# Performance work log

Measured on AMD Instinct MI355X. Metric: run time of the kernel, lower is better.

## Reference

```python
import jax, jax.numpy as jnp
import numpy as np

V, D, L, H, HD, FF, E, K, B, S = 32000, 768, 4, 12, 64, 2048, 8, 2, 2, 512
EPS = 1e-6
SCALE = HD ** -0.5


def rmsnorm(x, w):
    return w * x * jax.lax.rsqrt(jnp.mean(x * x, axis=-1, keepdims=True) + EPS)


def attention(x, wq, wk, wv, wo):
    # x: [B,S,D]
    q = jnp.einsum('bsd,de->bse', x, wq).reshape(B, S, H, HD)
    k = jnp.einsum('bsd,de->bse', x, wk).reshape(B, S, H, HD)
    v = jnp.einsum('bsd,de->bse', x, wv).reshape(B, S, H, HD)
    scores = jnp.einsum('bqhd,bkhd->bhqk', q, k) * SCALE
    a = jax.nn.softmax(scores, axis=-1)
    out = jnp.einsum('bhqk,bkhd->bqhd', a, v).reshape(B, S, D)
    return out @ wo


def moe(x, rw, gw, uw, dw):
    # x: [T,D]; rw: [D,E]; gw/uw: [E,D,FF]; dw: [E,FF,D]
    probs = jax.nn.softmax(x @ rw, axis=-1)            # [T,E]
    topv, topi = jax.lax.top_k(probs, K)               # [T,K]
    topv = topv / jnp.sum(topv, axis=-1, keepdims=True)
    combine = jnp.einsum('tke,tk->te', jax.nn.one_hot(topi, E, dtype=x.dtype), topv)  # [T,E]
    g = jnp.einsum('td,edf->etf', x, gw)               # [E,T,FF]
    u = jnp.einsum('td,edf->etf', x, uw)
    eo = jnp.einsum('etf,efd->etd', jax.nn.silu(g) * u, dw)  # [E,T,D]
    return jnp.einsum('etd,te->td', eo, combine)


def setup_inputs() -> dict:
    key = jax.random.key(0)
    ks = jax.random.split(key, 12)
    p = lambda k, shape: 0.02 * jax.random.normal(k, shape, jnp.float32)
    return {
        'input_ids': jax.random.randint(ks[0], (B, S), 0, V),
        'embed_tokens': p(ks[1], (V, D)),
        'embed_pos': p(ks[2], (S, D)),
        'wq': p(ks[3], (L, D, D)),
        'wk': p(ks[4], (L, D, D)),
        'wv': p(ks[5], (L, D, D)),
        'wo': p(ks[6], (L, D, D)),
        'norm1_w': jnp.ones((L, D), jnp.float32),
        'norm2_w': jnp.ones((L, D), jnp.float32),
        'router_w': p(ks[7], (L, D, E)),
        'gate_w': p(ks[8], (L, E, D, FF)),
        'up_w': p(ks[9], (L, E, D, FF)),
        'down_w': p(ks[10], (L, E, FF, D)),
        'final_norm_w': jnp.ones((D,), jnp.float32),
        'lm_head_w': p(ks[11], (D, V)),
    }


def reference(input_ids, embed_tokens, embed_pos, wq, wk, wv, wo, norm1_w, norm2_w,
              router_w, gate_w, up_w, down_w, final_norm_w, lm_head_w):
    x = embed_tokens[input_ids] + embed_pos[None, :, :]   # [B,S,D]
    for l in range(L):
        x = x + attention(rmsnorm(x, norm1_w[l]), wq[l], wk[l], wv[l], wo[l])
        t = rmsnorm(x, norm2_w[l]).reshape(-1, D)
        x = x + moe(t, router_w[l], gate_w[l], up_w[l], down_w[l]).reshape(B, S, D)
    logits = rmsnorm(x, final_norm_w) @ lm_head_w        # [B,S,V]
    return logits
```

## Files before the change

kernel.cpp:

```cpp
#include <hip/hip_runtime.h>
#include <math.h>

#define TT   1024
#define DM   768
#define NH   12
#define HD   64
#define FFD  2048
#define NE   8
#define SQ   512
#define NB   2
#define NL   4
#define NV   32000
#define REPS 1e-6f
#define QB   16
#define LMC  3200

typedef float f32x4 __attribute__((ext_vector_type(4)));
typedef short s16x8 __attribute__((ext_vector_type(8)));

__device__ __forceinline__ float b2f(ushort u) {
  return __uint_as_float(((unsigned)u) << 16);
}
__device__ __forceinline__ ushort f2b(float f) {
  unsigned i = __float_as_uint(f);
  return (ushort)((i + 0x7FFFu + ((i >> 16) & 1u)) >> 16);
}

__global__ __launch_bounds__(256) void k_embed(const int* __restrict__ ids,
    const float* __restrict__ tok, const float* __restrict__ pos, float* __restrict__ x) {
  int t = blockIdx.x; int s = t % SQ; int id = ids[t];
  for (int d = threadIdx.x; d < DM; d += 256)
    x[t * DM + d] = tok[(size_t)id * DM + d] + pos[s * DM + d];
}

__global__ __launch_bounds__(64) void k_router(const float* __restrict__ xn,
    const float* __restrict__ rw, int* __restrict__ topi, float* __restrict__ topw,
    int* __restrict__ posb, int* __restrict__ slot, int* __restrict__ counts) {
  int t = blockIdx.x, l = threadIdx.x;
  float acc[NE] = {};
  for (int d = l; d < DM; d += 64) {
    float xv = xn[t * DM + d];
    const float* r = &rw[d * NE];
#pragma unroll
    for (int e = 0; e < NE; ++e) acc[e] += xv * r[e];
  }
#pragma unroll
  for (int off = 32; off > 0; off >>= 1)
#pragma unroll
    for (int e = 0; e < NE; ++e) acc[e] += __shfl_down(acc[e], off, 64);
  if (l == 0) {
    float mx = acc[0];
#pragma unroll
    for (int e = 1; e < NE; ++e) mx = fmaxf(mx, acc[e]);
    float p[NE], sum = 0.f;
#pragma unroll
    for (int e = 0; e < NE; ++e) { p[e] = expf(acc[e] - mx); sum += p[e]; }
#pragma unroll
    for (int e = 0; e < NE; ++e) p[e] /= sum;
    int i0 = 0;
    for (int e = 1; e < NE; ++e) if (p[e] > p[i0]) i0 = e;
    int i1 = (i0 == 0) ? 1 : 0;
    for (int e = 0; e < NE; ++e) if (e != i0 && p[e] > p[i1]) i1 = e;
    float w0 = p[i0], w1 = p[i1], inv = 1.f / (w0 + w1);
    w0 *= inv; w1 *= inv;
    int p0 = atomicAdd(&counts[i0], 1);
    int p1 = atomicAdd(&counts[i1], 1);
    topi[2 * t] = i0; topi[2 * t + 1] = i1;
    topw[2 * t] = w0; topw[2 * t + 1] = w1;
    posb[2 * t] = p0; posb[2 * t + 1] = p1;
    slot[i0 * TT + p0] = t; slot[i1 * TT + p1] = t;
  }
}

__global__ void k_zero8(int* c) { if (threadIdx.x < NE) c[threadIdx.x] = 0; }

__global__ void k_offsets(const int* __restrict__ counts, int* __restrict__ off) {
  int a = 0;
  for (int e = 0; e < NE; ++e) { off[e] = a; a += counts[e]; }
  off[NE] = a;
}

__global__ __launch_bounds__(256) void k_combine(const float* __restrict__ eo,
    const int* __restrict__ topi, const float* __restrict__ topw,
    const int* __restrict__ posb, const int* __restrict__ offs, float* __restrict__ x) {
  int t = blockIdx.x;
  int r0 = offs[topi[2 * t]] + posb[2 * t];
  int r1 = offs[topi[2 * t + 1]] + posb[2 * t + 1];
  float w0 = topw[2 * t], w1 = topw[2 * t + 1];
  for (int d = threadIdx.x; d < DM; d += 256)
    x[t * DM + d] += w0 * eo[(size_t)r0 * DM + d] + w1 * eo[(size_t)r1 * DM + d];
}

__global__ __launch_bounds__(256) void k_attn2(const float* __restrict__ qkv,
    float* __restrict__ O) {
  __shared__ float Qs[QB][64];
  __shared__ float KVs[128][68];
  __shared__ float sc[QB][516];
  __shared__ float red[256];
  __shared__ float mrow[QB], invr[QB];
  int qt = blockIdx.x, h = blockIdx.y, b = blockIdx.z;
  int tid = threadIdx.x;
  int q0 = qt * QB;
  const float* base = qkv + (size_t)(b * SQ) * (3 * DM);
  {
    int qi = tid >> 4, d4 = (tid & 15) * 4;
    *(float4*)&Qs[qi][d4] = *(const float4*)&base[(size_t)(q0 + qi) * (3 * DM) + h * HD + d4];
  }
  for (int kt = 0; kt < 4; ++kt) {
    __syncthreads();
    {
      int kk = tid >> 4, d4 = (tid & 15) * 4;
#pragma unroll
      for (int i = 0; i < 8; ++i)
        *(float4*)&KVs[kk + 16 * i][d4] =
            *(const float4*)&base[(size_t)(kt * 128 + kk + 16 * i) * (3 * DM) + DM + h * HD + d4];
    }
    __syncthreads();
    int q2 = tid >> 5, k4 = tid & 31;
    float a0[4] = {}, a1[4] = {};
#pragma unroll
    for (int i = 0; i < 16; ++i) {
      float4 qa = *(float4*)&Qs[2 * q2][4 * i];
      float4 qb = *(float4*)&Qs[2 * q2 + 1][4 * i];
#pragma unroll
      for (int j = 0; j < 4; ++j) {
        float4 kv = *(float4*)&KVs[k4 + 32 * j][4 * i];
        a0[j] += qa.x * kv.x + qa.y * kv.y + qa.z * kv.z + qa.w * kv.w;
        a1[j] += qb.x * kv.x + qb.y * kv.y + qb.z * kv.z + qb.w * kv.w;
      }
    }
#pragma unroll
    for (int j = 0; j < 4; ++j) {
      sc[2 * q2][kt * 128 + 32 * j + k4] = a0[j] * 0.125f;
      sc[2 * q2 + 1][kt * 128 + 32 * j + k4] = a1[j] * 0.125f;
    }
  }
  __syncthreads();
  int row = tid & 15, seg = tid >> 4;
  float m = -1e30f;
  for (int i = 0; i < 32; ++i) m = fmaxf(m, sc[row][seg + 16 * i]);
  red[tid] = m; __syncthreads();
  if (tid < QB) {
    float mm = red[tid];
#pragma unroll
    for (int j = 1; j < 16; ++j) mm = fmaxf(mm, red[tid + 16 * j]);
    mrow[tid] = mm;
  }
  __syncthreads();
  m = mrow[row];
  float s = 0.f;
  for (int i = 0; i < 32; ++i) {
    int c = seg + 16 * i;
    float e = expf(sc[row][c] - m);
    sc[row][c] = e; s += e;
  }
  red[tid] = s; __syncthreads();
  if (tid < QB) {
    float ss = red[tid];
#pragma unroll
    for (int j = 1; j < 16; ++j) ss += red[tid + 16 * j];
    invr[tid] = 1.0f / ss;
  }
  float4 o = {0.f, 0.f, 0.f, 0.f};
  int q = tid >> 4, d4 = (tid & 15) * 4;
  for (int vt = 0; vt < 4; ++vt) {
    __syncthreads();
    {
      int kk = tid >> 4, dd = (tid & 15) * 4;
#pragma unroll
      for (int i = 0; i < 8; ++i)
        *(float4*)&KVs[kk + 16 * i][dd] =
            *(const float4*)&base[(size_t)(vt * 128 + kk + 16 * i) * (3 * DM) + 2 * DM + h * HD + dd];
    }
    __syncthreads();
    for (int kk = 0; kk < 128; ++kk) {
      float w = sc[q][vt * 128 + kk];
      float4 v = *(float4*)&KVs[kk][d4];
      o.x += w * v.x; o.y += w * v.y; o.z += w * v.z; o.w += w * v.w;
    }
  }
  float iv = invr[q];
  o.x *= iv; o.y *= iv; o.z *= iv; o.w *= iv;
  *(float4*)&O[(size_t)(b * SQ + q0 + q) * DM + h * HD + d4] = o;
}

__global__ __launch_bounds__(256) void k_rmsnorm_sb(const float* __restrict__ x,
    const float* __restrict__ w, float* __restrict__ y,
    ushort* __restrict__ yh, ushort* __restrict__ yl) {
  __shared__ float red[256];
  int t = blockIdx.x, tid = threadIdx.x;
  float ss = 0.f;
  for (int d = tid; d < DM; d += 256) { float v = x[t * DM + d]; ss += v * v; }
  red[tid] = ss; __syncthreads();
  for (int s = 128; s > 0; s >>= 1) { if (tid < s) red[tid] += red[tid + s]; __syncthreads(); }
  float inv = 1.0f / sqrtf(red[0] / (float)DM + REPS);
  for (int d = tid; d < DM; d += 256) {
    float v = w[d] * x[t * DM + d] * inv;
    ushort h = f2b(v);
    y[t * DM + d] = v;
    yh[t * DM + d] = h;
    yl[t * DM + d] = f2b(v - b2f(h));
  }
}

__global__ __launch_bounds__(256) void k_split(const float* __restrict__ in,
    ushort* __restrict__ oh, ushort* __restrict__ ol) {
  int t = blockIdx.x;
  for (int d = threadIdx.x; d < DM; d += 256) {
    float v = in[(size_t)t * DM + d];
    ushort h = f2b(v);
    oh[(size_t)t * DM + d] = h;
    ol[(size_t)t * DM + d] = f2b(v - b2f(h));
  }
}

__global__ __launch_bounds__(256) void k_rmsnorm_b(const float* __restrict__ x,
    const float* __restrict__ w, ushort* __restrict__ y) {
  __shared__ float red[256];
  int t = blockIdx.x, tid = threadIdx.x;
  float ss = 0.f;
  for (int d = tid; d < DM; d += 256) { float v = x[t * DM + d]; ss += v * v; }
  red[tid] = ss; __syncthreads();
  for (int s = 128; s > 0; s >>= 1) { if (tid < s) red[tid] += red[tid + s]; __syncthreads(); }
  float inv = 1.0f / sqrtf(red[0] / (float)DM + REPS);
  for (int d = tid; d < DM; d += 256)
    y[t * DM + d] = f2b(w[d] * x[t * DM + d] * inv);
}

__global__ __launch_bounds__(256) void k_tconv(const float* __restrict__ in,
    ushort* __restrict__ out, int K, int ns, int mode) {
  __shared__ float tile[32][33];
  int n0 = blockIdx.x * 32, k0 = blockIdx.y * 32;
  int c = threadIdx.x & 31, rq = threadIdx.x >> 5;
#pragma unroll
  for (int rr = rq; rr < 32; rr += 8)
    tile[rr][c] = in[(size_t)(k0 + rr) * ns + n0 + c];
  __syncthreads();
#pragma unroll
  for (int rr = rq; rr < 32; rr += 8) {
    int n = n0 + rr;
    int orow = (mode == 0) ? n : (((n >> 4) << 5) + ((mode == 1) ? 0 : 16) + (n & 15));
    out[(size_t)orow * K + k0 + c] = f2b(tile[c][rr]);
  }
}

#define EPI_RES  1
#define EPI_F32  2
#define EPI_GU   3
#define EPI_DOWN 4
#define MODE_B   0
#define MODE_QKV 1
#define MODE_GU  2

template<int EPI, int RM>
__global__ __launch_bounds__(256) void k_gmm(
    const ushort* __restrict__ A, const ushort* __restrict__ Bt,
    ushort* __restrict__ Cb, float* __restrict__ Cf,
    int M, int K, int ldc, int e_arg,
    const int* __restrict__ slot, const int* __restrict__ counts,
    const int* __restrict__ offs) {
  (void)e_arg; (void)slot; (void)counts; (void)offs; (void)Cb;
  int cnt = M;
  int m0 = blockIdx.y * 128;
  if (m0 >= cnt) return;
  int n0 = blockIdx.x * 128;
  __shared__ __align__(16) ushort As[128 * 40];
  __shared__ __align__(16) ushort Bs[128 * 40];
  int tid = threadIdx.x;
  int lane = tid & 63;
  int wave = tid >> 6;
  int wr = wave >> 1, wc = wave & 1;
  int ar1 = tid >> 2, ar2 = ar1 + 64, kc = tid & 3;
  const ushort* Arow1 = A + (size_t)(m0 + ar1) * K;
  const ushort* Arow2 = A + (size_t)(m0 + ar2) * K;
  const ushort* Brow1 = Bt + (size_t)(n0 + ar1) * K;
  const ushort* Brow2 = Bt + (size_t)(n0 + ar2) * K;
  f32x4 zr = {0.f, 0.f, 0.f, 0.f};
  f32x4 acc[4][4];
#pragma unroll
  for (int i = 0; i < 4; ++i)
#pragma unroll
    for (int j = 0; j < 4; ++j) acc[i][j] = zr;
  int rl = lane & 15, g = lane >> 4;
  for (int k0 = 0; k0 < K; k0 += 32) {
    s16x8 va1 = *(const s16x8*)(Arow1 + k0 + kc * 8);
    s16x8 va2 = *(const s16x8*)(Arow2 + k0 + kc * 8);
    s16x8 vb1 = *(const s16x8*)(Brow1 + k0 + kc * 8);
    s16x8 vb2 = *(const s16x8*)(Brow2 + k0 + kc * 8);
    __syncthreads();
    *(s16x8*)&As[ar1 * 40 + kc * 8] = va1;
    *(s16x8*)&As[ar2 * 40 + kc * 8] = va2;
    *(s16x8*)&Bs[ar1 * 40 + kc * 8] = vb1;
    *(s16x8*)&Bs[ar2 * 40 + kc * 8] = vb2;
    __syncthreads();
    s16x8 av[4], bv[4];
#pragma unroll
    for (int mi = 0; mi < 4; ++mi)
      av[mi] = *(const s16x8*)&As[(wr * 64 + mi * 16 + rl) * 40 + g * 8];
#pragma unroll
    for (int ni = 0; ni < 4; ++ni)
      bv[ni] = *(const s16x8*)&Bs[(wc * 64 + ni * 16 + rl) * 40 + g * 8];
#pragma unroll
    for (int mi = 0; mi < 4; ++mi)
#pragma unroll
      for (int ni = 0; ni < 4; ++ni)
        acc[mi][ni] = __builtin_amdgcn_mfma_f32_16x16x32_bf16(av[mi], bv[ni], acc[mi][ni], 0, 0, 0);
  }
  int rg4 = (lane >> 4) * 4;
#pragma unroll
  for (int mi = 0; mi < 4; ++mi)
#pragma unroll
    for (int rg = 0; rg < 4; ++rg) {
      int rloc = m0 + wr * 64 + mi * 16 + rg4 + rg;
#pragma unroll
      for (int ni = 0; ni < 4; ++ni)
        Cf[(size_t)rloc * ldc + n0 + wc * 64 + ni * 16 + rl] = acc[mi][ni][rg];
    }
}

template<int BM, int BN, int MODE, int EPI, int RM, int SK, int NBX, int PREC>
__global__ __launch_bounds__(256) void k_gmm2(
    const ushort* __restrict__ Ah, const ushort* __restrict__ Al,
    const float* __restrict__ B0, const float* __restrict__ B1, const float* __restrict__ B2,
    long long bstride, ushort* __restrict__ Ch, ushort* __restrict__ Cl,
    float* __restrict__ Cf, float* __restrict__ Cf2,
    int M, int K, int ldb, int ldc,
    const int* __restrict__ slot, const int* __restrict__ counts,
    const int* __restrict__ offs) {
  constexpr int NEg  = (RM == 0) ? 1 : NE;
  constexpr int P    = NBX * NEg * SK;
  constexpr int Ppad = ((P + 7) / 8) * 8;
  int id = blockIdx.x;
  int m = id / Ppad, pp = id % Ppad;
  if (pp >= P) return;
  int e = pp / (NBX * SK);
  int rr = pp % (NBX * SK);
  int x = rr / SK, sk = rr % SK;

  int cnt = (RM == 0) ? M : counts[e];
  int m0 = m * BM;
  if (m0 >= cnt) return;
  int n0 = x * BN;
  int off = (RM == 0) ? 0 : offs[e];
  int KK = K / SK, kbeg = sk * KK;

  constexpr int WM = (BM == 128) ? 64 : ((BN == 128) ? 64 : 32);
  constexpr int WN = (BM == 128) ? 64 : 32;
  constexpr int MI = WM / 16, NI = WN / 16;

  __shared__ __align__(16) ushort Ahs[BM * 40];
  __shared__ __align__(16) ushort Als[(PREC == 2) ? BM * 40 : 16];
  __shared__ __align__(16) ushort Bhs[BN * 40];
  __shared__ __align__(16) ushort Bls[(PREC == 2) ? BN * 40 : 16];

  int tid = threadIdx.x;
  int wave = tid >> 6, lane = tid & 63;
  int wr, wc;
  if (BM == 128)      { wr = wave >> 1; wc = wave & 1; }
  else if (BN == 128) { wr = 0;         wc = wave;     }
  else                { wr = wave >> 1; wc = wave & 1; }
  int moff;
  if (BM == 64 && BN == 128) moff = 0; else moff = wr * ((BM == 128) ? 64 : 32);
  int noff = wc * WN;

  int arA = tid >> 2, kcA = tid & 3;
  int ar1 = tid >> 2, ar2 = ar1 + 64;
  size_t aoff1 = 0, aoff2 = 0;
  if (BM == 64) {
    int rowi;
    if (RM == 0)      rowi = m0 + arA;
    else if (RM == 1) rowi = slot[e * TT + min(m0 + arA, cnt - 1)];
    else              rowi = off + min(m0 + arA, cnt - 1);
    aoff1 = (size_t)rowi * K;
  } else {
    if (RM == 0) {
      aoff1 = (size_t)(m0 + ar1) * K;
      aoff2 = (size_t)(m0 + ar2) * K;
    } else if (RM == 1) {
      aoff1 = (size_t)slot[e * TT + min(m0 + ar1, cnt - 1)] * K;
      aoff2 = (size_t)slot[e * TT + min(m0 + ar2, cnt - 1)] * K;
    } else {
      aoff1 = (size_t)(off + min(m0 + ar1, cnt - 1)) * K;
      aoff2 = (size_t)(off + min(m0 + ar2, cnt - 1)) * K;
    }
  }

  int rB = tid & 63, ko = tid >> 6;
  auto bcol = [&](int r) -> const float* {
    if (MODE == MODE_QKV) {
      int mat = x / (NBX / 3);
      const float* Bm = (mat == 0) ? B0 : ((mat == 1) ? B1 : B2);
      return Bm + (x % (NBX / 3)) * BN + r;
    } else if (MODE == MODE_GU) {
      const float* Bg = B0 + (size_t)e * bstride;
      const float* Bu = B1 + (size_t)e * bstride;
      return ((((r) >> 4) & 1) ? Bu : Bg) + x * (BN / 2) + ((((r) >> 5) << 4) | ((r) & 15));
    }
    return B0 + (size_t)e * bstride + n0 + r;
  };
  const float* bs0 = bcol(rB);
  const float* bs1 = (BN == 128) ? bcol(rB + 64) : nullptr;

  s16x8 rah1, rah2, ral1, ral2;
  float vb0[8], vb1[8];

  auto loadA = [&](int kk) {
    if (BM == 64) {
      rah1 = *(const s16x8*)(Ah + aoff1 + kbeg + kk + kcA * 8);
      if (PREC == 2) ral1 = *(const s16x8*)(Al + aoff1 + kbeg + kk + kcA * 8);
    } else {
      rah1 = *(const s16x8*)(Ah + aoff1 + kbeg + kk + kcA * 8);
      rah2 = *(const s16x8*)(Ah + aoff2 + kbeg + kk + kcA * 8);
      if (PREC == 2) {
        ral1 = *(const s16x8*)(Al + aoff1 + kbeg + kk + kcA * 8);
        ral2 = *(const s16x8*)(Al + aoff2 + kbeg + kk + kcA * 8);
      }
    }
  };
  auto loadB = [&](int kk) {
#pragma unroll
    for (int i = 0; i < 8; ++i)
      vb0[i] = bs0[(size_t)(kbeg + kk + ko * 8 + i) * ldb];
    if (BN == 128) {
#pragma unroll
      for (int i = 0; i < 8; ++i)
        vb1[i] = bs1[(size_t)(kbeg + kk + ko * 8 + i) * ldb];
    }
  };
  auto storeLDS = [&]() {
    if (BM == 64) {
      *(s16x8*)&Ahs[arA * 40 + kcA * 8] = rah1;
      if (PREC == 2) *(s16x8*)&Als[arA * 40 + kcA * 8] = ral1;
    } else {
      *(s16x8*)&Ahs[ar1 * 40 + kcA * 8] = rah1;
      *(s16x8*)&Ahs[ar2 * 40 + kcA * 8] = rah2;
      if (PREC == 2) {
        *(s16x8*)&Als[ar1 * 40 + kcA * 8] = ral1;
        *(s16x8*)&Als[ar2 * 40 + kcA * 8] = ral2;
      }
    }
    s16x8 h0, l0;
#pragma unroll
    for (int i = 0; i < 8; ++i) {
      ushort h = f2b(vb0[i]);
      h0[i] = (short)h;
      if (PREC == 2) l0[i] = (short)f2b(vb0[i] - b2f(h));
    }
    *(s16x8*)&Bhs[rB * 40 + ko * 8] = h0;
    if (PREC == 2) *(s16x8*)&Bls[rB * 40 + ko * 8] = l0;
    if (BN == 128) {
      s16x8 h1, l1;
#pragma unroll
      for (int i = 0; i < 8; ++i) {
        ushort h = f2b(vb1[i]);
        h1[i] = (short)h;
        if (PREC == 2) l1[i] = (short)f2b(vb1[i] - b2f(h));
      }
      *(s16x8*)&Bhs[(rB + 64) * 40 + ko * 8] = h1;
      if (PREC == 2) *(s16x8*)&Bls[(rB + 64) * 40 + ko * 8] = l1;
    }
  };

  f32x4 zr = {0.f, 0.f, 0.f, 0.f};
  f32x4 acc[MI][NI];
#pragma unroll
  for (int i = 0; i < MI; ++i)
#pragma unroll
    for (int j = 0; j < NI; ++j) acc[i][j] = zr;

  int rl = lane & 15, g = lane >> 4;
  loadA(0); loadB(0);
  for (int k0 = 0; k0 < KK; k0 += 32) {
    __syncthreads();
    storeLDS();
    __syncthreads();
    if (k0 + 32 < KK) { loadA(k0 + 32); loadB(k0 + 32); }
#pragma unroll
    for (int mi = 0; mi < MI; ++mi) {
      int ra = (moff + mi * 16 + rl) * 40 + g * 8;
      s16x8 avh = *(const s16x8*)&Ahs[ra];
      s16x8 avl;
      if (PREC == 2) avl = *(const s16x8*)&Als[ra];
#pragma unroll
      for (int ni = 0; ni < NI; ++ni) {
        int rb = (noff + ni * 16 + rl) * 40 + g * 8;
        s16x8 bvh = *(const s16x8*)&Bhs[rb];
        f32x4 a = acc[mi][ni];
        if (PREC == 2) {
          s16x8 bvl = *(const s16x8*)&Bls[rb];
          a = __builtin_amdgcn_mfma_f32_16x16x32_bf16(avl, bvh, a, 0, 0, 0);
          a = __builtin_amdgcn_mfma_f32_16x16x32_bf16(avh, bvl, a, 0, 0, 0);
        }
        a = __builtin_amdgcn_mfma_f32_16x16x32_bf16(avh, bvh, a, 0, 0, 0);
        acc[mi][ni] = a;
      }
    }
  }

  float* Cfx = (SK == 2 && sk == 1) ? Cf2 : Cf;
  int rg4 = (lane >> 4) * 4;
#pragma unroll
  for (int mi = 0; mi < MI; ++mi) {
#pragma unroll
    for (int rg = 0; rg < 4; ++rg) {
      int rloc = m0 + moff + mi * 16 + rg4 + rg;
      if ((EPI == EPI_GU || EPI == EPI_DOWN) && rloc >= cnt) continue;
      if (EPI == EPI_GU) {
        float gv = acc[mi][0][rg], uv = acc[mi][1][rg];
        float hv = gv / (1.f + __expf(-gv)) * uv;
        int fq = (n0 + noff) >> 5;
        size_t ix = (size_t)(off + rloc) * ldc + fq * 16 + rl;
        ushort h = f2b(hv);
        Ch[ix] = h;
        Cl[ix] = f2b(hv - b2f(h));
      } else if (EPI == EPI_RES) {
#pragma unroll
        for (int ni = 0; ni < NI; ++ni) {
          size_t ix = (size_t)rloc * ldc + n0 + noff + ni * 16 + rl;
          Cf[ix] += acc[mi][ni][rg];
        }
      } else if (EPI == EPI_F32) {
#pragma unroll
        for (int ni = 0; ni < NI; ++ni)
          Cfx[(size_t)rloc * ldc + n0 + noff + ni * 16 + rl] = acc[mi][ni][rg];
      } else {
#pragma unroll
        for (int ni = 0; ni < NI; ++ni)
          Cfx[(size_t)(off + rloc) * ldc + n0 + noff + ni * 16 + rl] = acc[mi][ni][rg];
      }
    }
  }
}

extern "C" void kernel_launch(void* const* d_in, const int* in_sizes, int n_in,
                              void* d_out, int out_size, void* d_ws, size_t ws_size,
                              hipStream_t stream) {
  (void)in_sizes; (void)n_in; (void)out_size; (void)ws_size;
  const int*   ids = (const int*)d_in[0];
  const float* tok = (const float*)d_in[1];
  const float* pos = (const float*)d_in[2];
  const float* wq  = (const float*)d_in[3];
  const float* wk  = (const float*)d_in[4];
  const float* wv  = (const float*)d_in[5];
  const float* wo  = (const float*)d_in[6];
  const float* n1w = (const float*)d_in[7];
  const float* n2w = (const float*)d_in[8];
  const float* rw  = (const float*)d_in[9];
  const float* gw  = (const float*)d_in[10];
  const float* uw  = (const float*)d_in[11];
  const float* dw  = (const float*)d_in[12];
  const float* fnw = (const float*)d_in[13];
  const float* lmw = (const float*)d_in[14];
  float* out = (float*)d_out;

  char* p = (char*)d_ws;
  auto alloc = [&](size_t bytes) { char* r = p; p += (bytes + 255) & ~(size_t)255; return r; };
  float*  x    = (float*)alloc((size_t)TT * DM * 4);
  float*  xn   = (float*)alloc((size_t)TT * DM * 4);
  ushort* xh   = (ushort*)alloc((size_t)TT * DM * 2);
  ushort* xl   = (ushort*)alloc((size_t)TT * DM * 2);
  float*  qkv  = (float*)alloc((size_t)TT * 3 * DM * 4);
  float*  ao   = (float*)alloc((size_t)TT * DM * 4);
  ushort* aoh  = (ushort*)alloc((size_t)TT * DM * 2);
  ushort* aol  = (ushort*)alloc((size_t)TT * DM * 2);
  ushort* Hh   = (ushort*)alloc((size_t)2 * TT * FFD * 2);
  ushort* Hl   = (ushort*)alloc((size_t)2 * TT * FFD * 2);
  float*  eo   = (float*)alloc((size_t)2 * TT * DM * 4);
  float*  topw = (float*)alloc((size_t)2 * TT * 4);
  int* topi    = (int*)alloc((size_t)2 * TT * 4);
  int* posb    = (int*)alloc((size_t)2 * TT * 4);
  int* slot    = (int*)alloc((size_t)NE * TT * 4);
  int* counts  = (int*)alloc(256);
  int* offs    = (int*)alloc(256);
  ushort* wlm  = (ushort*)alloc((size_t)LMC * DM * 2);
  ushort* xnb  = (ushort*)alloc((size_t)TT * DM * 2);

  k_embed<<<TT, 256, 0, stream>>>(ids, tok, pos, x);
  for (int l = 0; l < NL; ++l) {
    k_rmsnorm_sb<<<TT, 256, 0, stream>>>(x, n1w + l * DM, xn, xh, xl);
    k_gmm2<64, 64, MODE_QKV, EPI_F32, 0, 1, 36, 2><<<16 * 40, 256, 0, stream>>>(
        xh, xl, wq + (size_t)l * DM * DM, wk + (size_t)l * DM * DM, wv + (size_t)l * DM * DM,
        0, nullptr, nullptr, qkv, nullptr, TT, DM, DM, 3 * DM, nullptr, nullptr, nullptr);
    k_attn2<<<dim3(SQ / QB, NH, NB), 256, 0, stream>>>(qkv, ao);
    k_split<<<TT, 256, 0, stream>>>(ao, aoh, aol);
    k_gmm2<64, 64, MODE_B, EPI_RES, 0, 1, 12, 2><<<16 * 16, 256, 0, stream>>>(
        aoh, aol, wo + (size_t)l * DM * DM, nullptr, nullptr,
        0, nullptr, nullptr, x, nullptr, TT, DM, DM, DM, nullptr, nullptr, nullptr);

    k_rmsnorm_sb<<<TT, 256, 0, stream>>>(x, n2w + l * DM, xn, xh, xl);
    k_zero8<<<1, 64, 0, stream>>>(counts);
    k_router<<<TT, 64, 0, stream>>>(xn, rw + (size_t)l * DM * NE, topi, topw, posb, slot, counts);
    k_offsets<<<1, 1, 0, stream>>>(counts, offs);
    k_gmm2<64, 128, MODE_GU, EPI_GU, 1, 1, 32, 2><<<16 * 256, 256, 0, stream>>>(
        xh, xl, gw + (size_t)l * NE * DM * FFD, uw + (size_t)l * NE * DM * FFD, nullptr,
        (long long)DM * FFD, Hh, Hl, nullptr, nullptr, TT, DM, FFD, FFD, slot, counts, offs);
    k_gmm2<64, 64, MODE_B, EPI_DOWN, 2, 1, 12, 2><<<16 * 96, 256, 0, stream>>>(
        Hh, Hl, dw + (size_t)l * NE * FFD * DM, nullptr, nullptr,
        (long long)FFD * DM, nullptr, nullptr, eo, nullptr, TT, FFD, DM, DM, slot, counts, offs);
    k_combine<<<TT, 256, 0, stream>>>(eo, topi, topw, posb, offs, x);
  }

  k_rmsnorm_b<<<TT, 256, 0, stream>>>(x, fnw, xnb);
  for (int c = 0; c < NV / LMC; ++c) {
    k_tconv<<<dim3(LMC / 32, 24), 256, 0, stream>>>(lmw + c * LMC, wlm, DM, NV, 0);
    k_gmm<EPI_F32, 0><<<dim3(LMC / 128, 8), 256, 0, stream>>>(
        xnb, wlm, nullptr, out + c * LMC, TT, DM, NV, 0, nullptr, nullptr, nullptr);
  }
}
```

Baseline: 1.650 ms.

## Fuse split into attention, drop tiny kernels, single-pass LM head GEMM

The attention kernel now writes bf16 hi/lo outputs directly, so the separate split kernel and its fp32 round-trip go away. The counts zeroing moves into the rmsnorm kernel, and the expert offsets are computed inline from counts inside the GEMM and combine kernels, removing two single-block launches. The LM head drops the 10-chunk transpose-convert plus GEMM loop in favour of one k_gmm2 launch that reads the fp32 weights directly in single-bf16 precision, with a column-major block decode. Split-K support is removed from k_gmm2.

```diff
diff --git a/kernel.cpp b/kernel.cpp
--- a/kernel.cpp
+++ b/kernel.cpp
@@ -13,7 +13,6 @@
 #define NV   32000
 #define REPS 1e-6f
 #define QB   16
-#define LMC  3200
 
 typedef float f32x4 __attribute__((ext_vector_type(4)));
 typedef short s16x8 __attribute__((ext_vector_type(8)));
@@ -72,27 +71,22 @@
   }
 }
 
-__global__ void k_zero8(int* c) { if (threadIdx.x < NE) c[threadIdx.x] = 0; }
-
-__global__ void k_offsets(const int* __restrict__ counts, int* __restrict__ off) {
-  int a = 0;
-  for (int e = 0; e < NE; ++e) { off[e] = a; a += counts[e]; }
-  off[NE] = a;
-}
-
 __global__ __launch_bounds__(256) void k_combine(const float* __restrict__ eo,
     const int* __restrict__ topi, const float* __restrict__ topw,
-    const int* __restrict__ posb, const int* __restrict__ offs, float* __restrict__ x) {
+    const int* __restrict__ posb, const int* __restrict__ counts, float* __restrict__ x) {
   int t = blockIdx.x;
-  int r0 = offs[topi[2 * t]] + posb[2 * t];
-  int r1 = offs[topi[2 * t + 1]] + posb[2 * t + 1];
+  int pre[NE]; int a = 0;
+#pragma unroll
+  for (int e = 0; e < NE; ++e) { pre[e] = a; a += counts[e]; }
+  int r0 = pre[topi[2 * t]] + posb[2 * t];
+  int r1 = pre[topi[2 * t + 1]] + posb[2 * t + 1];
   float w0 = topw[2 * t], w1 = topw[2 * t + 1];
   for (int d = threadIdx.x; d < DM; d += 256)
     x[t * DM + d] += w0 * eo[(size_t)r0 * DM + d] + w1 * eo[(size_t)r1 * DM + d];
 }
 
 __global__ __launch_bounds__(256) void k_attn2(const float* __restrict__ qkv,
-    float* __restrict__ O) {
+    ushort* __restrict__ aoh, ushort* __restrict__ aol) {
   __shared__ float Qs[QB][64];
   __shared__ float KVs[128][68];
   __shared__ float sc[QB][516];
@@ -180,15 +174,22 @@
     }
   }
   float iv = invr[q];
-  o.x *= iv; o.y *= iv; o.z *= iv; o.w *= iv;
-  *(float4*)&O[(size_t)(b * SQ + q0 + q) * DM + h * HD + d4] = o;
+  size_t ob = (size_t)(b * SQ + q0 + q) * DM + h * HD + d4;
+  float ov[4] = {o.x * iv, o.y * iv, o.z * iv, o.w * iv};
+#pragma unroll
+  for (int j = 0; j < 4; ++j) {
+    ushort hh = f2b(ov[j]);
+    aoh[ob + j] = hh;
+    aol[ob + j] = f2b(ov[j] - b2f(hh));
+  }
 }
 
 __global__ __launch_bounds__(256) void k_rmsnorm_sb(const float* __restrict__ x,
     const float* __restrict__ w, float* __restrict__ y,
-    ushort* __restrict__ yh, ushort* __restrict__ yl) {
+    ushort* __restrict__ yh, ushort* __restrict__ yl, int* __restrict__ zc) {
   __shared__ float red[256];
   int t = blockIdx.x, tid = threadIdx.x;
+  if (zc && t == 0 && tid < NE) zc[tid] = 0;
   float ss = 0.f;
   for (int d = tid; d < DM; d += 256) { float v = x[t * DM + d]; ss += v * v; }
   red[tid] = ss; __syncthreads();
@@ -203,17 +204,6 @@
   }
 }
 
-__global__ __launch_bounds__(256) void k_split(const float* __restrict__ in,
-    ushort* __restrict__ oh, ushort* __restrict__ ol) {
-  int t = blockIdx.x;
-  for (int d = threadIdx.x; d < DM; d += 256) {
-    float v = in[(size_t)t * DM + d];
-    ushort h = f2b(v);
-    oh[(size_t)t * DM + d] = h;
-    ol[(size_t)t * DM + d] = f2b(v - b2f(h));
-  }
-}
-
 __global__ __launch_bounds__(256) void k_rmsnorm_b(const float* __restrict__ x,
     const float* __restrict__ w, ushort* __restrict__ y) {
   __shared__ float red[256];
@@ -227,23 +217,6 @@
     y[t * DM + d] = f2b(w[d] * x[t * DM + d] * inv);
 }
 
-__global__ __launch_bounds__(256) void k_tconv(const float* __restrict__ in,
-    ushort* __restrict__ out, int K, int ns, int mode) {
-  __shared__ float tile[32][33];
-  int n0 = blockIdx.x * 32, k0 = blockIdx.y * 32;
-  int c = threadIdx.x & 31, rq = threadIdx.x >> 5;
-#pragma unroll
-  for (int rr = rq; rr < 32; rr += 8)
-    tile[rr][c] = in[(size_t)(k0 + rr) * ns + n0 + c];
-  __syncthreads();
-#pragma unroll
-  for (int rr = rq; rr < 32; rr += 8) {
-    int n = n0 + rr;
-    int orow = (mode == 0) ? n : (((n >> 4) << 5) + ((mode == 1) ? 0 : 16) + (n & 15));
-    out[(size_t)orow * K + k0 + c] = f2b(tile[c][rr]);
-  }
-}
-
 #define EPI_RES  1
 #define EPI_F32  2
 #define EPI_GU   3
@@ -252,97 +225,35 @@
 #define MODE_QKV 1
 #define MODE_GU  2
 
-template<int EPI, int RM>
-__global__ __launch_bounds__(256) void k_gmm(
-    const ushort* __restrict__ A, const ushort* __restrict__ Bt,
-    ushort* __restrict__ Cb, float* __restrict__ Cf,
-    int M, int K, int ldc, int e_arg,
-    const int* __restrict__ slot, const int* __restrict__ counts,
-    const int* __restrict__ offs) {
-  (void)e_arg; (void)slot; (void)counts; (void)offs; (void)Cb;
-  int cnt = M;
-  int m0 = blockIdx.y * 128;
-  if (m0 >= cnt) return;
-  int n0 = blockIdx.x * 128;
-  __shared__ __align__(16) ushort As[128 * 40];
-  __shared__ __align__(16) ushort Bs[128 * 40];
-  int tid = threadIdx.x;
-  int lane = tid & 63;
-  int wave = tid >> 6;
-  int wr = wave >> 1, wc = wave & 1;
-  int ar1 = tid >> 2, ar2 = ar1 + 64, kc = tid & 3;
-  const ushort* Arow1 = A + (size_t)(m0 + ar1) * K;
-  const ushort* Arow2 = A + (size_t)(m0 + ar2) * K;
-  const ushort* Brow1 = Bt + (size_t)(n0 + ar1) * K;
-  const ushort* Brow2 = Bt + (size_t)(n0 + ar2) * K;
-  f32x4 zr = {0.f, 0.f, 0.f, 0.f};
-  f32x4 acc[4][4];
-#pragma unroll
-  for (int i = 0; i < 4; ++i)
-#pragma unroll
-    for (int j = 0; j < 4; ++j) acc[i][j] = zr;
-  int rl = lane & 15, g = lane >> 4;
-  for (int k0 = 0; k0 < K; k0 += 32) {
-    s16x8 va1 = *(const s16x8*)(Arow1 + k0 + kc * 8);
-    s16x8 va2 = *(const s16x8*)(Arow2 + k0 + kc * 8);
-    s16x8 vb1 = *(const s16x8*)(Brow1 + k0 + kc * 8);
-    s16x8 vb2 = *(const s16x8*)(Brow2 + k0 + kc * 8);
-    __syncthreads();
-    *(s16x8*)&As[ar1 * 40 + kc * 8] = va1;
-    *(s16x8*)&As[ar2 * 40 + kc * 8] = va2;
-    *(s16x8*)&Bs[ar1 * 40 + kc * 8] = vb1;
-    *(s16x8*)&Bs[ar2 * 40 + kc * 8] = vb2;
-    __syncthreads();
-    s16x8 av[4], bv[4];
-#pragma unroll
-    for (int mi = 0; mi < 4; ++mi)
-      av[mi] = *(const s16x8*)&As[(wr * 64 + mi * 16 + rl) * 40 + g * 8];
-#pragma unroll
-    for (int ni = 0; ni < 4; ++ni)
-      bv[ni] = *(const s16x8*)&Bs[(wc * 64 + ni * 16 + rl) * 40 + g * 8];
-#pragma unroll
-    for (int mi = 0; mi < 4; ++mi)
-#pragma unroll
-      for (int ni = 0; ni < 4; ++ni)
-        acc[mi][ni] = __builtin_amdgcn_mfma_f32_16x16x32_bf16(av[mi], bv[ni], acc[mi][ni], 0, 0, 0);
-  }
-  int rg4 = (lane >> 4) * 4;
-#pragma unroll
-  for (int mi = 0; mi < 4; ++mi)
-#pragma unroll
-    for (int rg = 0; rg < 4; ++rg) {
-      int rloc = m0 + wr * 64 + mi * 16 + rg4 + rg;
-#pragma unroll
-      for (int ni = 0; ni < 4; ++ni)
-        Cf[(size_t)rloc * ldc + n0 + wc * 64 + ni * 16 + rl] = acc[mi][ni][rg];
-    }
-}
-
-template<int BM, int BN, int MODE, int EPI, int RM, int SK, int NBX, int PREC>
+template<int BM, int BN, int MODE, int EPI, int RM, int NBX, int PREC, int DEC>
 __global__ __launch_bounds__(256) void k_gmm2(
     const ushort* __restrict__ Ah, const ushort* __restrict__ Al,
     const float* __restrict__ B0, const float* __restrict__ B1, const float* __restrict__ B2,
     long long bstride, ushort* __restrict__ Ch, ushort* __restrict__ Cl,
-    float* __restrict__ Cf, float* __restrict__ Cf2,
+    float* __restrict__ Cf,
     int M, int K, int ldb, int ldc,
-    const int* __restrict__ slot, const int* __restrict__ counts,
-    const int* __restrict__ offs) {
+    const int* __restrict__ slot, const int* __restrict__ counts) {
   constexpr int NEg  = (RM == 0) ? 1 : NE;
-  constexpr int P    = NBX * NEg * SK;
+  constexpr int P    = NBX * NEg;
   constexpr int Ppad = ((P + 7) / 8) * 8;
+  constexpr int MB   = TT / BM;
   int id = blockIdx.x;
-  int m = id / Ppad, pp = id % Ppad;
+  int m, pp;
+  if (DEC == 0) { m = id / Ppad; pp = id % Ppad; }
+  else          { m = id % MB;   pp = id / MB;   }
   if (pp >= P) return;
-  int e = pp / (NBX * SK);
-  int rr = pp % (NBX * SK);
-  int x = rr / SK, sk = rr % SK;
+  int e = pp / NBX;
+  int x = pp % NBX;
 
   int cnt = (RM == 0) ? M : counts[e];
   int m0 = m * BM;
   if (m0 >= cnt) return;
   int n0 = x * BN;
-  int off = (RM == 0) ? 0 : offs[e];
-  int KK = K / SK, kbeg = sk * KK;
+  int off = 0;
+  if (RM != 0) {
+#pragma unroll
+    for (int i = 0; i < NE; ++i) if (i < e) off += counts[i];
+  }
 
   constexpr int WM = (BM == 128) ? 64 : ((BN == 128) ? 64 : 32);
   constexpr int WN = (BM == 128) ? 64 : 32;
@@ -406,25 +317,25 @@
 
   auto loadA = [&](int kk) {
     if (BM == 64) {
-      rah1 = *(const s16x8*)(Ah + aoff1 + kbeg + kk + kcA * 8);
-      if (PREC == 2) ral1 = *(const s16x8*)(Al + aoff1 + kbeg + kk + kcA * 8);
+      rah1 = *(const s16x8*)(Ah + aoff1 + kk + kcA * 8);
+      if (PREC == 2) ral1 = *(const s16x8*)(Al + aoff1 + kk + kcA * 8);
     } else {
-      rah1 = *(const s16x8*)(Ah + aoff1 + kbeg + kk + kcA * 8);
-      rah2 = *(const s16x8*)(Ah + aoff2 + kbeg + kk + kcA * 8);
+      rah1 = *(const s16x8*)(Ah + aoff1 + kk + kcA * 8);
+      rah2 = *(const s16x8*)(Ah + aoff2 + kk + kcA * 8);
       if (PREC == 2) {
-        ral1 = *(const s16x8*)(Al + aoff1 + kbeg + kk + kcA * 8);
-        ral2 = *(const s16x8*)(Al + aoff2 + kbeg + kk + kcA * 8);
+        ral1 = *(const s16x8*)(Al + aoff1 + kk + kcA * 8);
+        ral2 = *(const s16x8*)(Al + aoff2 + kk + kcA * 8);
       }
     }
   };
   auto loadB = [&](int kk) {
 #pragma unroll
     for (int i = 0; i < 8; ++i)
-      vb0[i] = bs0[(size_t)(kbeg + kk + ko * 8 + i) * ldb];
+      vb0[i] = bs0[(size_t)(kk + ko * 8 + i) * ldb];
     if (BN == 128) {
 #pragma unroll
       for (int i = 0; i < 8; ++i)
-        vb1[i] = bs1[(size_t)(kbeg + kk + ko * 8 + i) * ldb];
+        vb1[i] = bs1[(size_t)(kk + ko * 8 + i) * ldb];
     }
   };
   auto storeLDS = [&]() {
@@ -470,11 +381,11 @@
 
   int rl = lane & 15, g = lane >> 4;
   loadA(0); loadB(0);
-  for (int k0 = 0; k0 < KK; k0 += 32) {
+  for (int k0 = 0; k0 < K; k0 += 32) {
     __syncthreads();
     storeLDS();
     __syncthreads();
-    if (k0 + 32 < KK) { loadA(k0 + 32); loadB(k0 + 32); }
+    if (k0 + 32 < K) { loadA(k0 + 32); loadB(k0 + 32); }
 #pragma unroll
     for (int mi = 0; mi < MI; ++mi) {
       int ra = (moff + mi * 16 + rl) * 40 + g * 8;
@@ -497,7 +408,6 @@
     }
   }
 
-  float* Cfx = (SK == 2 && sk == 1) ? Cf2 : Cf;
   int rg4 = (lane >> 4) * 4;
 #pragma unroll
   for (int mi = 0; mi < MI; ++mi) {
@@ -522,11 +432,11 @@
       } else if (EPI == EPI_F32) {
 #pragma unroll
         for (int ni = 0; ni < NI; ++ni)
-          Cfx[(size_t)rloc * ldc + n0 + noff + ni * 16 + rl] = acc[mi][ni][rg];
+          Cf[(size_t)rloc * ldc + n0 + noff + ni * 16 + rl] = acc[mi][ni][rg];
       } else {
 #pragma unroll
         for (int ni = 0; ni < NI; ++ni)
-          Cfx[(size_t)(off + rloc) * ldc + n0 + noff + ni * 16 + rl] = acc[mi][ni][rg];
+          Cf[(size_t)(off + rloc) * ldc + n0 + noff + ni * 16 + rl] = acc[mi][ni][rg];
       }
     }
   }
@@ -560,7 +470,6 @@
   ushort* xh   = (ushort*)alloc((size_t)TT * DM * 2);
   ushort* xl   = (ushort*)alloc((size_t)TT * DM * 2);
   float*  qkv  = (float*)alloc((size_t)TT * 3 * DM * 4);
-  float*  ao   = (float*)alloc((size_t)TT * DM * 4);
   ushort* aoh  = (ushort*)alloc((size_t)TT * DM * 2);
   ushort* aol  = (ushort*)alloc((size_t)TT * DM * 2);
   ushort* Hh   = (ushort*)alloc((size_t)2 * TT * FFD * 2);
@@ -571,39 +480,32 @@
   int* posb    = (int*)alloc((size_t)2 * TT * 4);
   int* slot    = (int*)alloc((size_t)NE * TT * 4);
   int* counts  = (int*)alloc(256);
-  int* offs    = (int*)alloc(256);
-  ushort* wlm  = (ushort*)alloc((size_t)LMC * DM * 2);
   ushort* xnb  = (ushort*)alloc((size_t)TT * DM * 2);
 
   k_embed<<<TT, 256, 0, stream>>>(ids, tok, pos, x);
   for (int l = 0; l < NL; ++l) {
-    k_rmsnorm_sb<<<TT, 256, 0, stream>>>(x, n1w + l * DM, xn, xh, xl);
-    k_gmm2<64, 64, MODE_QKV, EPI_F32, 0, 1, 36, 2><<<16 * 40, 256, 0, stream>>>(
+    k_rmsnorm_sb<<<TT, 256, 0, stream>>>(x, n1w + l * DM, xn, xh, xl, nullptr);
+    k_gmm2<64, 64, MODE_QKV, EPI_F32, 0, 36, 2, 0><<<16 * 40, 256, 0, stream>>>(
         xh, xl, wq + (size_t)l * DM * DM, wk + (size_t)l * DM * DM, wv + (size_t)l * DM * DM,
-        0, nullptr, nullptr, qkv, nullptr, TT, DM, DM, 3 * DM, nullptr, nullptr, nullptr);
-    k_attn2<<<dim3(SQ / QB, NH, NB), 256, 0, stream>>>(qkv, ao);
-    k_split<<<TT, 256, 0, stream>>>(ao, aoh, aol);
-    k_gmm2<64, 64, MODE_B, EPI_RES, 0, 1, 12, 2><<<16 * 16, 256, 0, stream>>>(
+        0, nullptr, nullptr, qkv, TT, DM, DM, 3 * DM, nullptr, nullptr);
+    k_attn2<<<dim3(SQ / QB, NH, NB), 256, 0, stream>>>(qkv, aoh, aol);
+    k_gmm2<64, 64, MODE_B, EPI_RES, 0, 12, 2, 0><<<16 * 16, 256, 0, stream>>>(
         aoh, aol, wo + (size_t)l * DM * DM, nullptr, nullptr,
-        0, nullptr, nullptr, x, nullptr, TT, DM, DM, DM, nullptr, nullptr, nullptr);
-
-    k_rmsnorm_sb<<<TT, 256, 0, stream>>>(x, n2w + l * DM, xn, xh, xl);
-    k_zero8<<<1, 64, 0, stream>>>(counts);
+        0, nullptr, nullptr, x, TT, DM, DM, DM, nullptr, nullptr);
+
+    k_rmsnorm_sb<<<TT, 256, 0, stream>>>(x, n2w + l * DM, xn, xh, xl, counts);
     k_router<<<TT, 64, 0, stream>>>(xn, rw + (size_t)l * DM * NE, topi, topw, posb, slot, counts);
-    k_offsets<<<1, 1, 0, stream>>>(counts, offs);
-    k_gmm2<64, 128, MODE_GU, EPI_GU, 1, 1, 32, 2><<<16 * 256, 256, 0, stream>>>(
+    k_gmm2<64, 128, MODE_GU, EPI_GU, 1, 32, 2, 0><<<16 * 256, 256, 0, stream>>>(
         xh, xl, gw + (size_t)l * NE * DM * FFD, uw + (size_t)l * NE * DM * FFD, nullptr,
-        (long long)DM * FFD, Hh, Hl, nullptr, nullptr, TT, DM, FFD, FFD, slot, counts, offs);
-    k_gmm2<64, 64, MODE_B, EPI_DOWN, 2, 1, 12, 2><<<16 * 96, 256, 0, stream>>>(
+        (long long)DM * FFD, Hh, Hl, nullptr, TT, DM, FFD, FFD, slot, counts);
+    k_gmm2<64, 64, MODE_B, EPI_DOWN, 2, 12, 2, 0><<<16 * 96, 256, 0, stream>>>(
         Hh, Hl, dw + (size_t)l * NE * FFD * DM, nullptr, nullptr,
-        (long long)FFD * DM, nullptr, nullptr, eo, nullptr, TT, FFD, DM, DM, slot, counts, offs);
-    k_combine<<<TT, 256, 0, stream>>>(eo, topi, topw, posb, offs, x);
+        (long long)FFD * DM, nullptr, nullptr, eo, TT, FFD, DM, DM, nullptr, counts);
+    k_combine<<<TT, 256, 0, stream>>>(eo, topi, topw, posb, counts, x);
   }
 
   k_rmsnorm_b<<<TT, 256, 0, stream>>>(x, fnw, xnb);
-  for (int c = 0; c < NV / LMC; ++c) {
-    k_tconv<<<dim3(LMC / 32, 24), 256, 0, stream>>>(lmw + c * LMC, wlm, DM, NV, 0);
-    k_gmm<EPI_F32, 0><<<dim3(LMC / 128, 8), 256, 0, stream>>>(
-        xnb, wlm, nullptr, out + c * LMC, TT, DM, NV, 0, nullptr, nullptr, nullptr);
-  }
-}
+  k_gmm2<64, 128, MODE_B, EPI_F32, 0, 250, 1, 1><<<16 * 256, 256, 0, stream>>>(
+      xnb, nullptr, lmw, nullptr, nullptr,
+      0, nullptr, nullptr, out, TT, DM, NV, NV, nullptr, nullptr);
+}
```

Measured after the change: 1.486 ms. -9.9%, faster.
